# Kernel tuning notes

Hardware: AMD Instinct MI355X
Metric: run time of the kernel (lower is better)

Reference implementation:

```python
import jax, jax.numpy as jnp
import numpy as np

N = 50000
E = 1600000
F_IN = 3
C = 40

def _linear_params(key, fan_in, fan_out):
    k1, k2 = jax.random.split(key)
    bound = 1.0 / np.sqrt(fan_in)
    W = jax.random.uniform(k1, (fan_in, fan_out), jnp.float32, -bound, bound)
    b = jax.random.uniform(k2, (fan_out,), jnp.float32, -bound, bound)
    return W, b

def setup_inputs() -> dict:
    key = jax.random.key(0)
    ks = jax.random.split(key, 9)
    x = jax.random.normal(ks[0], (N, F_IN), jnp.float32)
    pos = jax.random.normal(ks[1], (N, 3), jnp.float32)
    edge_index = jax.random.randint(ks[2], (2, E), 0, N, jnp.int64)
    W1, b1 = _linear_params(ks[3], F_IN + 3, 64)   # local_nn layer 1
    W2, b2 = _linear_params(ks[4], 64, 64)          # local_nn layer 2
    W3, b3 = _linear_params(ks[5], 64, 128)         # global_nn layer 1
    W4, b4 = _linear_params(ks[6], 128, 1024)       # global_nn layer 2
    W5, b5 = _linear_params(ks[7], 1024, 64)        # global_nn layer 3
    Wf, bf = _linear_params(ks[8], 64, C)           # fc
    return {"x": x, "pos": pos, "edge_index": edge_index,
            "W1": W1, "b1": b1, "W2": W2, "b2": b2,
            "W3": W3, "b3": b3, "W4": W4, "b4": b4,
            "W5": W5, "b5": b5, "Wf": Wf, "bf": bf}

def reference(x, pos, edge_index, W1, b1, W2, b2, W3, b3, W4, b4, W5, b5, Wf, bf):
    # PyG PointNetConv: add self-loops by default
    loop = jnp.arange(N, dtype=edge_index.dtype)
    src = jnp.concatenate([edge_index[0], loop])  # j
    dst = jnp.concatenate([edge_index[1], loop])  # i
    # message: local_nn(concat(x_j, pos_j - pos_i))  -> [E+N, 64]
    msg_in = jnp.concatenate([x[src], pos[src] - pos[dst]], axis=1)
    h = jax.nn.relu(msg_in @ W1 + b1)
    h = h @ W2 + b2
    # max-aggregate to destination nodes
    agg = jax.ops.segment_max(h, dst, num_segments=N)
    # global_nn
    g = jax.nn.relu(agg @ W3 + b3)
    g = jax.nn.relu(g @ W4 + b4)
    g = g @ W5 + b5
    # trailing relu + fc + log_softmax
    out = jax.nn.relu(g) @ Wf + bf
    return jax.nn.log_softmax(out, axis=1)
```

## Files before the change

### kernel.cpp

```cpp
#include <hip/hip_runtime.h>
#include <cstddef>
#include <cmath>

typedef __attribute__((ext_vector_type(8))) short bf16x8;
typedef __attribute__((ext_vector_type(4))) float f32x4;

static __device__ __forceinline__ f32x4 mfma16(bf16x8 a, bf16x8 b, f32x4 c) {
    return __builtin_amdgcn_mfma_f32_16x16x32_bf16(a, b, c, 0, 0, 0);
}
static __device__ __forceinline__ unsigned short f2bf(float f) {
    unsigned int u = __float_as_uint(f);
    return (unsigned short)((u + 0x7FFFu + ((u >> 16) & 1u)) >> 16);
}

#define NBK 256
#define CAP 12288

__global__ __launch_bounds__(256) void k_bin(const int* __restrict__ ei, int E,
                                             unsigned int* __restrict__ gcur,
                                             unsigned int* __restrict__ pairs) {
    __shared__ unsigned int h[NBK];
    __shared__ unsigned int base[NBK];
    int tid = threadIdx.x;
    h[tid] = 0u;
    __syncthreads();
    int idx = blockIdx.x * 256 + tid;
    int e0 = idx * 4;
    unsigned int vals[4]; int bs[4]; unsigned int rk[4]; int cnt4 = 0;
    if (e0 + 3 < E) {
        int4 s = ((const int4*)ei)[idx];
        int4 d = ((const int4*)(ei + E))[idx];
        int sa[4] = {s.x, s.y, s.z, s.w};
        int da[4] = {d.x, d.y, d.z, d.w};
        cnt4 = 4;
#pragma unroll
        for (int j = 0; j < 4; ++j) {
            bs[j] = da[j] >> 8;
            vals[j] = (unsigned int)sa[j] | ((unsigned int)(da[j] & 255) << 16);
            rk[j] = atomicAdd(&h[bs[j]], 1u);
        }
    } else {
        for (int e = e0; e < E; ++e) {
            int j = cnt4++;
            int sv = ei[e], dv = ei[E + e];
            bs[j] = dv >> 8;
            vals[j] = (unsigned int)sv | ((unsigned int)(dv & 255) << 16);
            rk[j] = atomicAdd(&h[bs[j]], 1u);
        }
    }
    __syncthreads();
    unsigned int c = h[tid];
    base[tid] = c ? atomicAdd(&gcur[tid], c) : 0u;
    __syncthreads();
    for (int j = 0; j < cnt4; ++j) {
        unsigned int p = base[bs[j]] + rk[j];
        if (p < CAP) pairs[(size_t)bs[j] * CAP + p] = vals[j];
    }
}

__global__ __launch_bounds__(256) void k_build(const unsigned int* __restrict__ gcur,
                                               const unsigned int* __restrict__ pairs,
                                               unsigned int* __restrict__ list,
                                               unsigned int* __restrict__ off,
                                               unsigned int* __restrict__ deg, int N) {
    __shared__ unsigned int cntL[NBK];
    __shared__ unsigned int s[NBK];
    __shared__ unsigned int curL[NBK];
    int b = blockIdx.x, t = threadIdx.x;
    unsigned int gstart = (unsigned int)b * CAP;
    unsigned int m = min(gcur[b], (unsigned int)CAP);
    cntL[t] = 0u;
    __syncthreads();
    for (unsigned int i = t; i < m; i += 256u)
        atomicAdd(&cntL[(pairs[gstart + i] >> 16) & 255u], 1u);
    __syncthreads();
    unsigned int c = cntL[t];
    s[t] = c;
    __syncthreads();
    for (int d = 1; d < 256; d <<= 1) {
        unsigned int v = (t >= d) ? s[t - d] : 0u;
        __syncthreads();
        s[t] += v;
        __syncthreads();
    }
    unsigned int excl = s[t] - c;
    int dst = b * 256 + t;
    if (dst < N) { off[dst] = gstart + excl; deg[dst] = c; }
    curL[t] = excl;
    __syncthreads();
    for (unsigned int i = t; i < m; i += 256u) {
        unsigned int v = pairs[gstart + i];
        unsigned int p = atomicAdd(&curL[(v >> 16) & 255u], 1u);
        list[gstart + p] = v & 0xFFFFu;
    }
}

__global__ void k_convert(const float* __restrict__ W1, const float* __restrict__ W2,
                          const float* __restrict__ W3, const float* __restrict__ W4,
                          const float* __restrict__ W5,
                          unsigned short* __restrict__ W1bt, unsigned short* __restrict__ W2bt,
                          unsigned short* __restrict__ W3bt, unsigned short* __restrict__ W4bt,
                          unsigned short* __restrict__ W5ct) {
    int id = blockIdx.x * 256 + threadIdx.x;
    if (id < 2048) {
        int n = id >> 5, k = id & 31;
        W1bt[id] = (k < 6) ? f2bf(W1[k * 64 + n]) : (unsigned short)0;
    } else if (id < 2048 + 4096) {
        int t = id - 2048;
        int n = t >> 6, k = t & 63;
        W2bt[t] = f2bf(W2[k * 64 + n]);
    } else if (id < 6144 + 8192) {
        int t = id - 6144;
        int n = t >> 6, k = t & 63;
        W3bt[t] = f2bf(W3[k * 128 + n]);
    } else if (id < 14336 + 131072) {
        int t = id - 14336;
        int n = t >> 7, k = t & 127;
        W4bt[t] = f2bf(W4[k * 1024 + n]);
    } else if (id < 145408 + 65536) {
        int t = id - 145408;
        int ch = t >> 12, rem = t & 4095;
        int n = rem >> 6, kl = rem & 63;
        W5ct[t] = f2bf(W5[(ch * 64 + kl) * 64 + n]);
    }
}

#define TPB_E 256
#define EDGE_WPB 4
__global__ __launch_bounds__(TPB_E, 4) void edge_kernel(
    const float* __restrict__ x, const float* __restrict__ pos,
    const unsigned int* __restrict__ off, const unsigned int* __restrict__ deg,
    const unsigned int* __restrict__ list,
    const unsigned short* __restrict__ W1bt, const float* __restrict__ b1,
    const unsigned short* __restrict__ W2bt, const float* __restrict__ b2,
    float* __restrict__ agg, int N, int dstStride)
{
    __shared__ __align__(16) short Hs[4][16 * 72];

    int tid = threadIdx.x;
    int lane = tid & 63;
    int w = tid >> 6;
    int lm = lane & 15;
    int quad = lane >> 4;
    short* H = Hs[w];
    int dst0 = blockIdx.x * EDGE_WPB + w;

    bf16x8 B1f[4], B2f[4][2];
    float b1c[4], b2c[4];
#pragma unroll
    for (int nt = 0; nt < 4; ++nt) {
        B1f[nt] = *(const bf16x8*)&W1bt[(nt * 16 + lm) * 32 + quad * 8];
        B2f[nt][0] = *(const bf16x8*)&W2bt[(nt * 16 + lm) * 64 + quad * 8];
        B2f[nt][1] = *(const bf16x8*)&W2bt[(nt * 16 + lm) * 64 + 32 + quad * 8];
        b1c[nt] = b1[nt * 16 + lm];
        b2c[nt] = b2[nt * 16 + lm];
    }

    unsigned int o0P = 0u, dgP = 0u;
    if (dst0 < N) { o0P = off[dst0]; dgP = deg[dst0]; }

    for (int dst = dst0; dst < N; dst += dstStride) {
        unsigned int o0 = o0P;
        int ecnt = (int)dgP;
        int dn = dst + dstStride;
        if (dn < N) { o0P = off[dn]; dgP = deg[dn]; }

        int M = ecnt + 1;
        float pi0 = pos[dst * 3 + 0], pi1 = pos[dst * 3 + 1], pi2 = pos[dst * 3 + 2];

        float m0 = -INFINITY, m1 = -INFINITY, m2 = -INFINITY, m3 = -INFINITY;

        auto ldidx = [&](int base) -> int {
            int i = min(base + lm, M - 1);
            return (i == 0) ? dst : (int)list[o0 + i - 1];
        };

        float vx0 = 0.f, vx1 = 0.f, vx2 = 0.f, vq0 = 0.f, vq1 = 0.f, vq2 = 0.f;
        int sNext = dst;
        if (quad == 0) {
            int s0 = ldidx(0);
            vx0 = x[s0 * 3 + 0]; vx1 = x[s0 * 3 + 1]; vx2 = x[s0 * 3 + 2];
            vq0 = pos[s0 * 3 + 0]; vq1 = pos[s0 * 3 + 1]; vq2 = pos[s0 * 3 + 2];
            if (16 < M) sNext = ldidx(16);
        }

        for (int base = 0; base < M; base += 16) {
            float nx0 = vx0, nx1 = vx1, nx2 = vx2, nq0 = vq0, nq1 = vq1, nq2 = vq2;
            int sN2 = sNext;
            if (quad == 0) {
                nx0 = x[sNext * 3 + 0]; nx1 = x[sNext * 3 + 1]; nx2 = x[sNext * 3 + 2];
                nq0 = pos[sNext * 3 + 0]; nq1 = pos[sNext * 3 + 1]; nq2 = pos[sNext * 3 + 2];
                if (base + 32 < M) sN2 = ldidx(base + 32);
            }
            bf16x8 A = {0, 0, 0, 0, 0, 0, 0, 0};
            if (quad == 0) {
                A[0] = (short)f2bf(vx0);
                A[1] = (short)f2bf(vx1);
                A[2] = (short)f2bf(vx2);
                A[3] = (short)f2bf(vq0 - pi0);
                A[4] = (short)f2bf(vq1 - pi1);
                A[5] = (short)f2bf(vq2 - pi2);
            }
#pragma unroll
            for (int nt = 0; nt < 4; ++nt) {
                f32x4 c = {0.f, 0.f, 0.f, 0.f};
                c = mfma16(A, B1f[nt], c);
#pragma unroll
                for (int r = 0; r < 4; ++r) {
                    float v = fmaxf(c[r] + b1c[nt], 0.f);
                    H[(quad * 4 + r) * 72 + nt * 16 + lm] = (short)f2bf(v);
                }
            }
            bf16x8 A2a = *(const bf16x8*)&H[lm * 72 + quad * 8];
            bf16x8 A2b = *(const bf16x8*)&H[lm * 72 + 32 + quad * 8];
            {
                f32x4 c = {0.f, 0.f, 0.f, 0.f};
                c = mfma16(A2a, B2f[0][0], c); c = mfma16(A2b, B2f[0][1], c);
                m0 = fmaxf(m0, fmaxf(fmaxf(c[0], c[1]), fmaxf(c[2], c[3])));
            }
            {
                f32x4 c = {0.f, 0.f, 0.f, 0.f};
                c = mfma16(A2a, B2f[1][0], c); c = mfma16(A2b, B2f[1][1], c);
                m1 = fmaxf(m1, fmaxf(fmaxf(c[0], c[1]), fmaxf(c[2], c[3])));
            }
            {
                f32x4 c = {0.f, 0.f, 0.f, 0.f};
                c = mfma16(A2a, B2f[2][0], c); c = mfma16(A2b, B2f[2][1], c);
                m2 = fmaxf(m2, fmaxf(fmaxf(c[0], c[1]), fmaxf(c[2], c[3])));
            }
            {
                f32x4 c = {0.f, 0.f, 0.f, 0.f};
                c = mfma16(A2a, B2f[3][0], c); c = mfma16(A2b, B2f[3][1], c);
                m3 = fmaxf(m3, fmaxf(fmaxf(c[0], c[1]), fmaxf(c[2], c[3])));
            }
            vx0 = nx0; vx1 = nx1; vx2 = nx2; vq0 = nq0; vq1 = nq1; vq2 = nq2;
            sNext = sN2;
        }

        m0 = fmaxf(m0, __shfl_xor(m0, 16, 64)); m0 = fmaxf(m0, __shfl_xor(m0, 32, 64));
        m1 = fmaxf(m1, __shfl_xor(m1, 16, 64)); m1 = fmaxf(m1, __shfl_xor(m1, 32, 64));
        m2 = fmaxf(m2, __shfl_xor(m2, 16, 64)); m2 = fmaxf(m2, __shfl_xor(m2, 32, 64));
        m3 = fmaxf(m3, __shfl_xor(m3, 16, 64)); m3 = fmaxf(m3, __shfl_xor(m3, 32, 64));

        float mv = (quad == 0) ? m0 : (quad == 1) ? m1 : (quad == 2) ? m2 : m3;
        agg[(size_t)dst * 64 + lane] = mv + b2c[quad];
    }
}

#define NNODE 64
__global__ __launch_bounds__(512, 4) void node_kernel(
    const float* __restrict__ agg,
    const unsigned short* __restrict__ W3bt, const float* __restrict__ b3,
    const unsigned short* __restrict__ W4bt, const float* __restrict__ b4,
    const unsigned short* __restrict__ W5ct, const float* __restrict__ b5,
    const float* __restrict__ Wf, const float* __restrict__ bf,
    float* __restrict__ out, int N)
{
    __shared__ __align__(16) char smem[79872];
    short* G1s = (short*)smem;
    float* G3f = (float*)smem;
    short* G2s = (short*)(smem + 17408);
    short* Wb4 = (short*)(smem + 26624);
    short* Wb5 = (short*)(smem + 61440);
    float* os  = (float*)(smem + 26624);

    int tid = threadIdx.x;
    int lane = tid & 63;
    int wm = tid >> 6;
    int m = wm & 3;
    int h = wm >> 2;
    int lm = lane & 15;
    int quad = lane >> 4;
    int n0 = blockIdx.x * NNODE;

    int4 s4a, s4b, s5;
    auto stage_load = [&](int ch) {
        const unsigned short* g4 = W4bt + (size_t)ch * 8192;
        s4a = *(const int4*)(g4 + tid * 8);
        s4b = *(const int4*)(g4 + (tid + 512) * 8);
        s5  = *(const int4*)(W5ct + (size_t)ch * 4096 + tid * 8);
    };
    auto stage_store = [&](int buf) {
        short* d4 = Wb4 + buf * 8704;
        *(int4*)&d4[(tid >> 4) * 136 + (tid & 15) * 8] = s4a;
        int v1 = tid + 512;
        *(int4*)&d4[(v1 >> 4) * 136 + (v1 & 15) * 8] = s4b;
        short* d5 = Wb5 + buf * 4608;
        *(int4*)&d5[(tid >> 3) * 72 + (tid & 7) * 8] = s5;
    };

    stage_load(0);
    stage_store(0);

    {
        int arow = min(n0 + m * 16 + lm, N - 1);
        bf16x8 A3[2];
#pragma unroll
        for (int f = 0; f < 2; ++f) {
            const float* p = agg + (size_t)arow * 64 + f * 32 + quad * 8;
            float4 u = *(const float4*)p;
            float4 v = *(const float4*)(p + 4);
            bf16x8 t;
            t[0] = (short)f2bf(u.x); t[1] = (short)f2bf(u.y);
            t[2] = (short)f2bf(u.z); t[3] = (short)f2bf(u.w);
            t[4] = (short)f2bf(v.x); t[5] = (short)f2bf(v.y);
            t[6] = (short)f2bf(v.z); t[7] = (short)f2bf(v.w);
            A3[f] = t;
        }
#pragma unroll
        for (int nt2 = 0; nt2 < 4; ++nt2) {
            int nt = h * 4 + nt2;
            const unsigned short* wb = W3bt + (nt * 16 + lm) * 64 + quad * 8;
            f32x4 c = {0.f, 0.f, 0.f, 0.f};
            c = mfma16(A3[0], *(const bf16x8*)wb, c);
            c = mfma16(A3[1], *(const bf16x8*)(wb + 32), c);
            float bias = b3[nt * 16 + lm];
#pragma unroll
            for (int r = 0; r < 4; ++r) {
                float v = fmaxf(c[r] + bias, 0.f);
                G1s[(m * 16 + quad * 4 + r) * 136 + nt * 16 + lm] = (short)f2bf(v);
            }
        }
    }

    f32x4 acc3[4];
#pragma unroll
    for (int nt = 0; nt < 4; ++nt) {
        float b = (h == 0) ? b5[nt * 16 + lm] : 0.f;
        acc3[nt][0] = b; acc3[nt][1] = b; acc3[nt][2] = b; acc3[nt][3] = b;
    }

    __syncthreads();

    bf16x8 A4[4];
#pragma unroll
    for (int f = 0; f < 4; ++f)
        A4[f] = *(const bf16x8*)&G1s[(m * 16 + lm) * 136 + f * 32 + quad * 8];

    for (int ch = 0; ch < 16; ++ch) {
        int buf = ch & 1;
        if (ch < 15) stage_load(ch + 1);
        __builtin_amdgcn_sched_barrier(0);

        const short* w4b = Wb4 + buf * 8704;
        const short* w5b = Wb5 + buf * 4608;

#pragma unroll
        for (int nt2 = 0; nt2 < 2; ++nt2) {
            int nt = h * 2 + nt2;
            const short* wb = w4b + (nt * 16 + lm) * 136 + quad * 8;
            f32x4 c = {0.f, 0.f, 0.f, 0.f};
            c = mfma16(A4[0], *(const bf16x8*)wb, c);
            c = mfma16(A4[1], *(const bf16x8*)(wb + 32), c);
            c = mfma16(A4[2], *(const bf16x8*)(wb + 64), c);
            c = mfma16(A4[3], *(const bf16x8*)(wb + 96), c);
            float bias = b4[ch * 64 + nt * 16 + lm];
#pragma unroll
            for (int r = 0; r < 4; ++r) {
                float v = fmaxf(c[r] + bias, 0.f);
                G2s[(m * 16 + quad * 4 + r) * 72 + nt * 16 + lm] = (short)f2bf(v);
            }
        }
        bf16x8 A5 = *(const bf16x8*)&G2s[(m * 16 + lm) * 72 + h * 32 + quad * 8];
#pragma unroll
        for (int nt = 0; nt < 4; ++nt) {
            const short* wb = w5b + (nt * 16 + lm) * 72 + h * 32 + quad * 8;
            acc3[nt] = mfma16(A5, *(const bf16x8*)wb, acc3[nt]);
        }
        if (ch < 15) stage_store(buf ^ 1);
        __syncthreads();
    }

    if (h == 0) {
#pragma unroll
        for (int nt = 0; nt < 4; ++nt)
#pragma unroll
            for (int r = 0; r < 4; ++r)
                G3f[(m * 16 + quad * 4 + r) * 68 + nt * 16 + lm] = acc3[nt][r];
    }
    __syncthreads();
    if (h == 1) {
#pragma unroll
        for (int nt = 0; nt < 4; ++nt)
#pragma unroll
            for (int r = 0; r < 4; ++r) {
                int idx = (m * 16 + quad * 4 + r) * 68 + nt * 16 + lm;
                G3f[idx] = fmaxf(G3f[idx] + acc3[nt][r], 0.f);
            }
    }
    __syncthreads();

    for (int idx = tid; idx < NNODE * 40; idx += 512) {
        int ln = idx / 40;
        int c = idx - ln * 40;
        float o = bf[c];
#pragma unroll 4
        for (int j = 0; j < 64; ++j)
            o = fmaf(G3f[ln * 68 + j], Wf[j * 40 + c], o);
        os[ln * 41 + c] = o;
    }
    __syncthreads();

    if (tid < NNODE && n0 + tid < N) {
        int ln = tid;
        float mx = os[ln * 41 + 0];
#pragma unroll
        for (int c = 1; c < 40; ++c) mx = fmaxf(mx, os[ln * 41 + c]);
        float s = 0.f;
#pragma unroll
        for (int c = 0; c < 40; ++c) s += expf(os[ln * 41 + c] - mx);
        float ls = logf(s) + mx;
        float* op = out + (size_t)(n0 + tid) * 40;
#pragma unroll
        for (int c = 0; c < 40; ++c) op[c] = os[ln * 41 + c] - ls;
    }
}

extern "C" void kernel_launch(void* const* d_in, const int* in_sizes, int n_in,
                              void* d_out, int out_size, void* d_ws, size_t ws_size,
                              hipStream_t stream) {
    const float* x   = (const float*)d_in[0];
    const float* pos = (const float*)d_in[1];
    const int*   ei  = (const int*)d_in[2];
    const float* W1  = (const float*)d_in[3];
    const float* b1  = (const float*)d_in[4];
    const float* W2  = (const float*)d_in[5];
    const float* b2  = (const float*)d_in[6];
    const float* W3  = (const float*)d_in[7];
    const float* b3  = (const float*)d_in[8];
    const float* W4  = (const float*)d_in[9];
    const float* b4  = (const float*)d_in[10];
    const float* W5  = (const float*)d_in[11];
    const float* b5  = (const float*)d_in[12];
    const float* Wf  = (const float*)d_in[13];
    const float* bf  = (const float*)d_in[14];
    float* out = (float*)d_out;

    int Nn = in_sizes[0] / 3;
    int E  = in_sizes[2] / 2;

    char* w = (char*)d_ws;
    size_t p = 0;
    auto take = [&](size_t bytes) { size_t q = p; p = (p + bytes + 255) & ~size_t(255); return (void*)(w + q); };
    unsigned int*   off   = (unsigned int*)take((size_t)Nn * 4);
    unsigned int*   deg   = (unsigned int*)take((size_t)Nn * 4);
    unsigned int*   gcur  = (unsigned int*)take(NBK * 4);
    unsigned int*   list  = (unsigned int*)take((size_t)NBK * CAP * 4);
    float*          agg   = (float*)take((size_t)Nn * 64 * 4);
    unsigned int*   pairs = (unsigned int*)agg;
    unsigned short* W1bt = (unsigned short*)take(2048 * 2);
    unsigned short* W2bt = (unsigned short*)take(4096 * 2);
    unsigned short* W3bt = (unsigned short*)take(8192 * 2);
    unsigned short* W4bt = (unsigned short*)take(131072 * 2);
    unsigned short* W5ct = (unsigned short*)take(65536 * 2);

    hipMemsetAsync(gcur, 0, NBK * 4, stream);
    k_convert<<<(2048 + 4096 + 8192 + 131072 + 65536 + 255) / 256, 256, 0, stream>>>(
        W1, W2, W3, W4, W5, W1bt, W2bt, W3bt, W4bt, W5ct);

    int q4 = (E + 3) / 4;
    int gb = (q4 + 255) / 256;
    k_bin<<<gb, 256, 0, stream>>>(ei, E, gcur, pairs);
    int nb = (Nn + 255) >> 8;
    k_build<<<nb, 256, 0, stream>>>(gcur, pairs, list, off, deg, Nn);

    int totalWaves = (Nn + 3) / 4;
    int eBlocks = (totalWaves + EDGE_WPB - 1) / EDGE_WPB;
    int dstStride = eBlocks * EDGE_WPB;
    edge_kernel<<<eBlocks, TPB_E, 0, stream>>>(
        x, pos, off, deg, list, W1bt, b1, W2bt, b2, agg, Nn, dstStride);

    node_kernel<<<(Nn + NNODE - 1) / NNODE, 512, 0, stream>>>(
        agg, W3bt, b3, W4bt, b4, W5ct, b5, Wf, bf, out, Nn);
}
```

Before: 300.2 us.

## Precompute per-node first-layer projections and drop per-edge layer-1 MFMA

The first linear layer is split algebraically. A new prep kernel computes U = x·W1x + pos·W1p + b1 and V = pos·W1p for every node, so each edge's hidden activation becomes relu(U[src] - V[dst]). This removes the per-edge layer-1 MFMA, its LDS round trip, and the software prefetch of x/pos. In exchange each edge gathers a 256-byte fp32 U row instead of 24 bytes of x/pos, which adds memory traffic and two extra N×64 buffers. The prefetch of off/deg for the next destination is also dropped.

```diff
diff --git a/kernel.cpp b/kernel.cpp
--- a/kernel.cpp
+++ b/kernel.cpp
@@ -95,124 +95,111 @@
     }
 }
 
-__global__ void k_convert(const float* __restrict__ W1, const float* __restrict__ W2,
-                          const float* __restrict__ W3, const float* __restrict__ W4,
-                          const float* __restrict__ W5,
-                          unsigned short* __restrict__ W1bt, unsigned short* __restrict__ W2bt,
-                          unsigned short* __restrict__ W3bt, unsigned short* __restrict__ W4bt,
-                          unsigned short* __restrict__ W5ct) {
+__global__ void k_convert(const float* __restrict__ W2, const float* __restrict__ W3,
+                          const float* __restrict__ W4, const float* __restrict__ W5,
+                          unsigned short* __restrict__ W2bt, unsigned short* __restrict__ W3bt,
+                          unsigned short* __restrict__ W4bt, unsigned short* __restrict__ W5ct) {
     int id = blockIdx.x * 256 + threadIdx.x;
-    if (id < 2048) {
-        int n = id >> 5, k = id & 31;
-        W1bt[id] = (k < 6) ? f2bf(W1[k * 64 + n]) : (unsigned short)0;
-    } else if (id < 2048 + 4096) {
-        int t = id - 2048;
-        int n = t >> 6, k = t & 63;
-        W2bt[t] = f2bf(W2[k * 64 + n]);
-    } else if (id < 6144 + 8192) {
-        int t = id - 6144;
+    if (id < 4096) {
+        int n = id >> 6, k = id & 63;
+        W2bt[id] = f2bf(W2[k * 64 + n]);
+    } else if (id < 4096 + 8192) {
+        int t = id - 4096;
         int n = t >> 6, k = t & 63;
         W3bt[t] = f2bf(W3[k * 128 + n]);
-    } else if (id < 14336 + 131072) {
-        int t = id - 14336;
+    } else if (id < 12288 + 131072) {
+        int t = id - 12288;
         int n = t >> 7, k = t & 127;
         W4bt[t] = f2bf(W4[k * 1024 + n]);
-    } else if (id < 145408 + 65536) {
-        int t = id - 145408;
+    } else if (id < 143360 + 65536) {
+        int t = id - 143360;
         int ch = t >> 12, rem = t & 4095;
         int n = rem >> 6, kl = rem & 63;
         W5ct[t] = f2bf(W5[(ch * 64 + kl) * 64 + n]);
     }
 }
 
+__global__ __launch_bounds__(256) void k_prep(const float* __restrict__ x,
+                                              const float* __restrict__ pos,
+                                              const float* __restrict__ W1,
+                                              const float* __restrict__ b1,
+                                              float* __restrict__ Uw,
+                                              float* __restrict__ Vw, int N) {
+    int id = blockIdx.x * 256 + threadIdx.x;
+    if (id >= N * 64) return;
+    int n = id >> 6, f = id & 63;
+    float x0 = x[n * 3 + 0], x1 = x[n * 3 + 1], x2 = x[n * 3 + 2];
+    float p0 = pos[n * 3 + 0], p1 = pos[n * 3 + 1], p2 = pos[n * 3 + 2];
+    float v = p0 * W1[3 * 64 + f] + p1 * W1[4 * 64 + f] + p2 * W1[5 * 64 + f];
+    float u = x0 * W1[0 * 64 + f] + x1 * W1[1 * 64 + f] + x2 * W1[2 * 64 + f] + v + b1[f];
+    Uw[id] = u;
+    Vw[id] = v;
+}
+
 #define TPB_E 256
 #define EDGE_WPB 4
 __global__ __launch_bounds__(TPB_E, 4) void edge_kernel(
-    const float* __restrict__ x, const float* __restrict__ pos,
+    const float* __restrict__ Uw, const float* __restrict__ Vw,
     const unsigned int* __restrict__ off, const unsigned int* __restrict__ deg,
     const unsigned int* __restrict__ list,
-    const unsigned short* __restrict__ W1bt, const float* __restrict__ b1,
     const unsigned short* __restrict__ W2bt, const float* __restrict__ b2,
     float* __restrict__ agg, int N, int dstStride)
 {
-    __shared__ __align__(16) short Hs[4][16 * 72];
-
     int tid = threadIdx.x;
     int lane = tid & 63;
     int w = tid >> 6;
     int lm = lane & 15;
     int quad = lane >> 4;
-    short* H = Hs[w];
     int dst0 = blockIdx.x * EDGE_WPB + w;
 
-    bf16x8 B1f[4], B2f[4][2];
-    float b1c[4], b2c[4];
+    bf16x8 B2f[4][2];
+    float b2c[4];
 #pragma unroll
     for (int nt = 0; nt < 4; ++nt) {
-        B1f[nt] = *(const bf16x8*)&W1bt[(nt * 16 + lm) * 32 + quad * 8];
         B2f[nt][0] = *(const bf16x8*)&W2bt[(nt * 16 + lm) * 64 + quad * 8];
         B2f[nt][1] = *(const bf16x8*)&W2bt[(nt * 16 + lm) * 64 + 32 + quad * 8];
-        b1c[nt] = b1[nt * 16 + lm];
         b2c[nt] = b2[nt * 16 + lm];
     }
 
-    unsigned int o0P = 0u, dgP = 0u;
-    if (dst0 < N) { o0P = off[dst0]; dgP = deg[dst0]; }
-
     for (int dst = dst0; dst < N; dst += dstStride) {
-        unsigned int o0 = o0P;
-        int ecnt = (int)dgP;
-        int dn = dst + dstStride;
-        if (dn < N) { o0P = off[dn]; dgP = deg[dn]; }
-
-        int M = ecnt + 1;
-        float pi0 = pos[dst * 3 + 0], pi1 = pos[dst * 3 + 1], pi2 = pos[dst * 3 + 2];
+        unsigned int o0 = off[dst];
+        int M = (int)deg[dst] + 1;
+
+        const float* vrow = Vw + (size_t)dst * 64 + quad * 8;
+        float4 va = *(const float4*)(vrow);
+        float4 vb = *(const float4*)(vrow + 4);
+        float4 vc = *(const float4*)(vrow + 32);
+        float4 vd = *(const float4*)(vrow + 36);
 
         float m0 = -INFINITY, m1 = -INFINITY, m2 = -INFINITY, m3 = -INFINITY;
 
-        auto ldidx = [&](int base) -> int {
+        for (int base = 0; base < M; base += 16) {
             int i = min(base + lm, M - 1);
-            return (i == 0) ? dst : (int)list[o0 + i - 1];
-        };
-
-        float vx0 = 0.f, vx1 = 0.f, vx2 = 0.f, vq0 = 0.f, vq1 = 0.f, vq2 = 0.f;
-        int sNext = dst;
-        if (quad == 0) {
-            int s0 = ldidx(0);
-            vx0 = x[s0 * 3 + 0]; vx1 = x[s0 * 3 + 1]; vx2 = x[s0 * 3 + 2];
-            vq0 = pos[s0 * 3 + 0]; vq1 = pos[s0 * 3 + 1]; vq2 = pos[s0 * 3 + 2];
-            if (16 < M) sNext = ldidx(16);
-        }
-
-        for (int base = 0; base < M; base += 16) {
-            float nx0 = vx0, nx1 = vx1, nx2 = vx2, nq0 = vq0, nq1 = vq1, nq2 = vq2;
-            int sN2 = sNext;
-            if (quad == 0) {
-                nx0 = x[sNext * 3 + 0]; nx1 = x[sNext * 3 + 1]; nx2 = x[sNext * 3 + 2];
-                nq0 = pos[sNext * 3 + 0]; nq1 = pos[sNext * 3 + 1]; nq2 = pos[sNext * 3 + 2];
-                if (base + 32 < M) sN2 = ldidx(base + 32);
-            }
-            bf16x8 A = {0, 0, 0, 0, 0, 0, 0, 0};
-            if (quad == 0) {
-                A[0] = (short)f2bf(vx0);
-                A[1] = (short)f2bf(vx1);
-                A[2] = (short)f2bf(vx2);
-                A[3] = (short)f2bf(vq0 - pi0);
-                A[4] = (short)f2bf(vq1 - pi1);
-                A[5] = (short)f2bf(vq2 - pi2);
-            }
-#pragma unroll
-            for (int nt = 0; nt < 4; ++nt) {
-                f32x4 c = {0.f, 0.f, 0.f, 0.f};
-                c = mfma16(A, B1f[nt], c);
-#pragma unroll
-                for (int r = 0; r < 4; ++r) {
-                    float v = fmaxf(c[r] + b1c[nt], 0.f);
-                    H[(quad * 4 + r) * 72 + nt * 16 + lm] = (short)f2bf(v);
-                }
-            }
-            bf16x8 A2a = *(const bf16x8*)&H[lm * 72 + quad * 8];
-            bf16x8 A2b = *(const bf16x8*)&H[lm * 72 + 32 + quad * 8];
+            int s = (i == 0) ? dst : (int)list[o0 + i - 1];
+            const float* urow = Uw + (size_t)s * 64 + quad * 8;
+            float4 ua = *(const float4*)(urow);
+            float4 ub = *(const float4*)(urow + 4);
+            float4 uc = *(const float4*)(urow + 32);
+            float4 ud = *(const float4*)(urow + 36);
+
+            bf16x8 A2a, A2b;
+            A2a[0] = (short)f2bf(fmaxf(ua.x - va.x, 0.f));
+            A2a[1] = (short)f2bf(fmaxf(ua.y - va.y, 0.f));
+            A2a[2] = (short)f2bf(fmaxf(ua.z - va.z, 0.f));
+            A2a[3] = (short)f2bf(fmaxf(ua.w - va.w, 0.f));
+            A2a[4] = (short)f2bf(fmaxf(ub.x - vb.x, 0.f));
+            A2a[5] = (short)f2bf(fmaxf(ub.y - vb.y, 0.f));
+            A2a[6] = (short)f2bf(fmaxf(ub.z - vb.z, 0.f));
+            A2a[7] = (short)f2bf(fmaxf(ub.w - vb.w, 0.f));
+            A2b[0] = (short)f2bf(fmaxf(uc.x - vc.x, 0.f));
+            A2b[1] = (short)f2bf(fmaxf(uc.y - vc.y, 0.f));
+            A2b[2] = (short)f2bf(fmaxf(uc.z - vc.z, 0.f));
+            A2b[3] = (short)f2bf(fmaxf(uc.w - vc.w, 0.f));
+            A2b[4] = (short)f2bf(fmaxf(ud.x - vd.x, 0.f));
+            A2b[5] = (short)f2bf(fmaxf(ud.y - vd.y, 0.f));
+            A2b[6] = (short)f2bf(fmaxf(ud.z - vd.z, 0.f));
+            A2b[7] = (short)f2bf(fmaxf(ud.w - vd.w, 0.f));
+
             {
                 f32x4 c = {0.f, 0.f, 0.f, 0.f};
                 c = mfma16(A2a, B2f[0][0], c); c = mfma16(A2b, B2f[0][1], c);
@@ -233,8 +220,6 @@
                 c = mfma16(A2a, B2f[3][0], c); c = mfma16(A2b, B2f[3][1], c);
                 m3 = fmaxf(m3, fmaxf(fmaxf(c[0], c[1]), fmaxf(c[2], c[3])));
             }
-            vx0 = nx0; vx1 = nx1; vx2 = nx2; vq0 = nq0; vq1 = nq1; vq2 = nq2;
-            sNext = sN2;
         }
 
         m0 = fmaxf(m0, __shfl_xor(m0, 16, 64)); m0 = fmaxf(m0, __shfl_xor(m0, 32, 64));
@@ -448,15 +433,17 @@
     unsigned int*   list  = (unsigned int*)take((size_t)NBK * CAP * 4);
     float*          agg   = (float*)take((size_t)Nn * 64 * 4);
     unsigned int*   pairs = (unsigned int*)agg;
-    unsigned short* W1bt = (unsigned short*)take(2048 * 2);
+    float*          Uw    = (float*)take((size_t)Nn * 64 * 4);
+    float*          Vw    = (float*)take((size_t)Nn * 64 * 4);
     unsigned short* W2bt = (unsigned short*)take(4096 * 2);
     unsigned short* W3bt = (unsigned short*)take(8192 * 2);
     unsigned short* W4bt = (unsigned short*)take(131072 * 2);
     unsigned short* W5ct = (unsigned short*)take(65536 * 2);
 
     hipMemsetAsync(gcur, 0, NBK * 4, stream);
-    k_convert<<<(2048 + 4096 + 8192 + 131072 + 65536 + 255) / 256, 256, 0, stream>>>(
-        W1, W2, W3, W4, W5, W1bt, W2bt, W3bt, W4bt, W5ct);
+    k_convert<<<(4096 + 8192 + 131072 + 65536 + 255) / 256, 256, 0, stream>>>(
+        W2, W3, W4, W5, W2bt, W3bt, W4bt, W5ct);
+    k_prep<<<(Nn * 64 + 255) / 256, 256, 0, stream>>>(x, pos, W1, b1, Uw, Vw, Nn);
 
     int q4 = (E + 3) / 4;
     int gb = (q4 + 255) / 256;
@@ -468,7 +455,7 @@
     int eBlocks = (totalWaves + EDGE_WPB - 1) / EDGE_WPB;
     int dstStride = eBlocks * EDGE_WPB;
     edge_kernel<<<eBlocks, TPB_E, 0, stream>>>(
-        x, pos, off, deg, list, W1bt, b1, W2bt, b2, agg, Nn, dstStride);
+        Uw, Vw, off, deg, list, W2bt, b2, agg, Nn, dstStride);
 
     node_kernel<<<(Nn + NNODE - 1) / NNODE, 512, 0, stream>>>(
         agg, W3bt, b3, W4bt, b4, W5ct, b5, Wf, bf, out, Nn);
```

Result: slower. 332.3 us (+10.7%).
